# Kernel tuning notes

Measured on AMD Instinct MI355X. Metric: run time of the kernel, lower is better.

## Reference

```python
import jax, jax.numpy as jnp
import numpy as np

SX = 512; SY = 512; C = 3; NK = 10; R = 10
DT = 0.2; DD = 5; SIGMA = 0.65; THETA_A = 1.0; NPOW = 2


def setup_inputs() -> dict:
    rng = np.random.RandomState(0)
    r = rng.uniform(0.3, 1.0, NK).astype(np.float32)
    m = rng.uniform(0.05, 0.5, NK).astype(np.float32)
    s = rng.uniform(0.01, 0.18, NK).astype(np.float32)
    h = rng.uniform(0.2, 1.0, NK).astype(np.float32)
    a = rng.uniform(0.0, 1.0, (NK, 3)).astype(np.float32)
    w = rng.uniform(0.01, 0.5, (NK, 3)).astype(np.float32)
    b = rng.uniform(0.0, 1.0, (NK, 3)).astype(np.float32)
    # compute_kernel(): radial distance grid, ring sigmoid * sum-of-bumps ker_f, normalized
    mid = SX // 2
    x = np.linspace(-mid, mid, 2 * mid, dtype=np.float32)
    X, Y = np.meshgrid(x, x, indexing='ij')
    dist = np.sqrt(X ** 2 + Y ** 2)
    D = dist[:, :, None] / ((R + 15.0) * r)                      # (SX, SY, NK)
    ring = 1.0 / (1.0 + np.exp((D - 1.0) * 10.0))                # sigmoid(-(D-1)*10)
    bumps = (b * np.exp(-((D[..., None] - a) ** 2) / w)).sum(-1)  # ker_f(D, a, w, b)
    K = (ring * bumps).astype(np.float32)
    nK_ker = K / K.sum(axis=(0, 1), keepdims=True)               # (SX, SY, NK)
    # kernel -> source channel, and kernel -> target channel one-hot (c1 as matrix)
    c0 = np.array([0, 0, 0, 1, 1, 1, 2, 2, 2, 0], dtype=np.int32)
    tgt = np.array([0, 1, 2, 0, 1, 2, 0, 1, 2, 0], dtype=np.int32)
    c1_mat = np.zeros((NK, C), dtype=np.int32)
    c1_mat[np.arange(NK), tgt] = 1
    key = jax.random.key(0)
    A = jax.random.uniform(key, (SX, SY, C), dtype=jnp.float32)  # scale_init_state = 1
    return {"A": A, "nK_ker": jnp.asarray(nK_ker), "m": jnp.asarray(m),
            "s": jnp.asarray(s), "h": jnp.asarray(h),
            "c0": jnp.asarray(c0), "c1_mat": jnp.asarray(c1_mat)}


def _sobel(A):
    """A: (SX, SY, Cc) -> (SX, SY, 2, Cc), circular (toroidal) boundary."""
    def grad_ax(ax):
        sm_ax = 1 - ax
        sm = jnp.roll(A, 1, sm_ax) + 2.0 * A + jnp.roll(A, -1, sm_ax)  # [1,2,1] smoothing
        return (jnp.roll(sm, -1, ax) - jnp.roll(sm, 1, ax)) / 8.0       # central diff
    return jnp.stack([grad_ax(0), grad_ax(1)], axis=2)


def _flowlenia_step(A, nK_ker, m, s, h, c0, c1_mat):
    # FFT Lenia convolution
    fA = jnp.fft.fft2(A, axes=(0, 1))                              # (SX, SY, C) complex
    fK = jnp.fft.fft2(jnp.fft.fftshift(nK_ker, axes=(0, 1)), axes=(0, 1))
    U = jnp.real(jnp.fft.ifft2(fK * fA[:, :, c0], axes=(0, 1)))    # (SX, SY, NK)
    # growth * h, then gather-sum kernels into target channels (c1)
    U = (2.0 * jnp.exp(-((U - m) ** 2) / (2.0 * s ** 2)) - 1.0) * h
    U = jnp.einsum('xyk,kc->xyc', U, c1_mat.astype(U.dtype))       # (SX, SY, C)
    # flow field
    nabla_U = _sobel(U)                                            # (SX, SY, 2, C)
    nabla_A = _sobel(A.sum(-1, keepdims=True))                     # (SX, SY, 2, 1)
    alpha = jnp.clip((A[:, :, None, :] / THETA_A) ** NPOW, 0.0, 1.0)
    F = nabla_U * (1.0 - alpha) - nabla_A * alpha                  # (SX, SY, 2, C)
    # reintegration tracking (mass-conserving advection over (2*DD+1)^2 shifts)
    xs = jnp.arange(SX, dtype=A.dtype)
    ys = jnp.arange(SY, dtype=A.dtype)
    X, Y = jnp.meshgrid(xs, ys, indexing='ij')
    pos = jnp.stack([X, Y], axis=-1) + 0.5                         # (SX, SY, 2) cell centers
    ma = DD - SIGMA                                                # max flow magnitude
    mu = pos[..., None] + DT * jnp.clip(F, -ma, ma)                # (SX, SY, 2, C)
    shifts = jnp.array([(dx, dy) for dx in range(-DD, DD + 1)
                        for dy in range(-DD, DD + 1)], dtype=jnp.int32)
    clip_hi = min(1.0, 2.0 * SIGMA)
    inv_norm = 1.0 / (4.0 * SIGMA ** 2)

    def body(acc, sh):
        dx, dy = sh[0], sh[1]
        rA = jnp.roll(jnp.roll(A, dx, 0), dy, 1)
        rmu = jnp.roll(jnp.roll(mu, dx, 0), dy, 1)
        sz = 0.5 - jnp.abs(pos[..., None] - rmu) + SIGMA
        area = jnp.prod(jnp.clip(sz, 0.0, clip_hi), axis=2) * inv_norm  # (SX, SY, C)
        return acc + rA * area, None

    nA, _ = jax.lax.scan(body, jnp.zeros_like(A), shifts)
    return nA


def reference(A, nK_ker, m, s, h, c0, c1_mat):
    return _flowlenia_step(A, nK_ker, m, s, h, c0, c1_mat)
```

## Files before the change

kernel.cpp:

```cpp
#include <hip/hip_runtime.h>
#include <math.h>

#define NF 512
#define NF2 (NF * NF)
#define RPB 4
#define ROWLEN 580
#define PI_F 3.14159265358979323846f

#define LPAD(q) ((q) + ((q) >> 3))

__device__ inline float2 cadd(float2 a, float2 b) { return make_float2(a.x + b.x, a.y + b.y); }
__device__ inline float2 csub(float2 a, float2 b) { return make_float2(a.x - b.x, a.y - b.y); }
__device__ inline float2 cmul(float2 a, float2 b) {
    return make_float2(a.x * b.x - a.y * b.y, a.x * b.y + a.y * b.x);
}

__device__ inline void fft8(float2 x[8], float dsign) {
    const float s = 0.70710678118654752440f;
    float2 a0 = cadd(x[0], x[4]), a1 = cadd(x[1], x[5]);
    float2 a2 = cadd(x[2], x[6]), a3 = cadd(x[3], x[7]);
    float2 b0 = csub(x[0], x[4]), b1 = csub(x[1], x[5]);
    float2 b2 = csub(x[2], x[6]), b3 = csub(x[3], x[7]);
    b1 = cmul(b1, make_float2(s, dsign * s));
    b2 = make_float2(-dsign * b2.y, dsign * b2.x);
    b3 = cmul(b3, make_float2(-s, dsign * s));
    float2 c0 = cadd(a0, a2), c1 = cadd(a1, a3);
    float2 c2 = csub(a0, a2), c3 = csub(a1, a3);
    c3 = make_float2(-dsign * c3.y, dsign * c3.x);
    float2 d0 = cadd(b0, b2), d1 = cadd(b1, b3);
    float2 d2 = csub(b0, b2), d3 = csub(b1, b3);
    d3 = make_float2(-dsign * d3.y, dsign * d3.x);
    x[0] = cadd(c0, c1); x[4] = csub(c0, c1);
    x[2] = cadd(c2, c3); x[6] = csub(c2, c3);
    x[1] = cadd(d0, d1); x[5] = csub(d0, d1);
    x[3] = cadd(d2, d3); x[7] = csub(d2, d3);
}

__device__ inline void twiddle8(float2 x[8], float2 wb) {
    float2 tw = wb;
    x[1] = cmul(x[1], tw); tw = cmul(tw, wb);
    x[2] = cmul(x[2], tw); tw = cmul(tw, wb);
    x[3] = cmul(x[3], tw); tw = cmul(tw, wb);
    x[4] = cmul(x[4], tw); tw = cmul(tw, wb);
    x[5] = cmul(x[5], tw); tw = cmul(tw, wb);
    x[6] = cmul(x[6], tw); tw = cmul(tw, wb);
    x[7] = cmul(x[7], tw);
}

__device__ inline void fft512_regs(float2 x[8], int b, float2* bufA, float2* bufB,
                                   const float2* Wt, float dsign) {
    fft8(x, dsign);
    float2 wb0 = make_float2(Wt[b].x, dsign * Wt[b].y);
    twiddle8(x, wb0);
#pragma unroll
    for (int p = 0; p < 8; ++p) bufA[9 * b + p] = x[p];
    __syncthreads();
#pragma unroll
    for (int j = 0; j < 8; ++j) x[j] = bufA[LPAD(b + 64 * j)];
    fft8(x, dsign);
    int u = b >> 3, v = b & 7;
    float2 wb1 = make_float2(Wt[b & ~7].x, dsign * Wt[b & ~7].y);
    twiddle8(x, wb1);
    int base = u * 64 + v;
#pragma unroll
    for (int p = 0; p < 8; ++p) bufB[LPAD(base + 8 * p)] = x[p];
    __syncthreads();
#pragma unroll
    for (int j = 0; j < 8; ++j) x[j] = bufB[LPAD(b + 64 * j)];
    fft8(x, dsign);
}

#define FFT_PRE                                                    \
    __shared__ float2 SHA[RPB][ROWLEN];                            \
    __shared__ float2 SHB[RPB][ROWLEN];                            \
    __shared__ float2 Wt[512];                                     \
    int tid = threadIdx.x;                                         \
    int rr_ = tid >> 6, bb_ = tid & 63;                            \
    {                                                              \
        float sn, cs;                                              \
        sincosf((PI_F / 256.0f) * (float)tid, &sn, &cs);           \
        Wt[tid] = make_float2(cs, sn);                             \
        sincosf((PI_F / 256.0f) * (float)(tid + 256), &sn, &cs);   \
        Wt[tid + 256] = make_float2(cs, sn);                       \
    }

__global__ __launch_bounds__(256) void k_fwd_p1(const float* __restrict__ A,
                                                const float* __restrict__ K,
                                                float2* __restrict__ Z) {
    FFT_PRE
    int pl = blockIdx.y;
    const float* bre; int sre, cre;
    const float* bim; int sim, cim;
    switch (pl) {
        case 0: bre = A; sre = 3; cre = 0; bim = A; sim = 3; cim = 1; break;
        case 1: bre = A; sre = 3; cre = 2; bim = K; sim = 10; cim = 0; break;
        case 2: bre = K; sre = 10; cre = 1; bim = K; sim = 10; cim = 2; break;
        case 3: bre = K; sre = 10; cre = 3; bim = K; sim = 10; cim = 4; break;
        case 4: bre = K; sre = 10; cre = 5; bim = K; sim = 10; cim = 6; break;
        case 5: bre = K; sre = 10; cre = 7; bim = K; sim = 10; cim = 8; break;
        default: bre = K; sre = 10; cre = 9; bim = nullptr; sim = 0; cim = 0; break;
    }
    int x0 = blockIdx.x * RPB;
    int row = x0 + rr_;
    float2 x[8];
#pragma unroll
    for (int j = 0; j < 8; ++j) {
        int idx = (row << 9) + bb_ + 64 * j;
        float vr = bre[idx * sre + cre];
        float vi = bim ? bim[idx * sim + cim] : 0.0f;
        x[j] = make_float2(vr, vi);
    }
    __syncthreads();
    fft512_regs(x, bb_, &SHA[rr_][0], &SHB[rr_][0], Wt, -1.0f);
#pragma unroll
    for (int p2 = 0; p2 < 8; ++p2) SHA[rr_][LPAD(64 * p2 + bb_)] = x[p2];
    __syncthreads();
    for (int i = tid; i < RPB * NF; i += 256) {
        int r2 = i & (RPB - 1), ky = i >> 2;
        Z[(size_t)((pl << 9) + ky) * NF + x0 + r2] = SHA[r2][LPAD(ky)];
    }
}

__global__ __launch_bounds__(512) void k_rows_mul(const float2* __restrict__ Z,
                                                  const int* __restrict__ c0,
                                                  float2* __restrict__ tmpT) {
    __shared__ float2 RS[14][NF];
    __shared__ float2 SCA[8][ROWLEN];
    __shared__ float2 SCB[8][ROWLEN];
    __shared__ float2 Wt[512];
    int tid = threadIdx.x;
    int rr_ = tid >> 6, bb_ = tid & 63;
    {
        float sn, cs;
        sincosf((PI_F / 256.0f) * (float)tid, &sn, &cs);
        Wt[tid] = make_float2(cs, sn);
    }
    int b = blockIdx.x;
    bool selfm = (b == 0);
    int r1 = selfm ? 0 : b;
    int r2 = selfm ? 256 : NF - b;
    __syncthreads();

    for (int batch = 0; batch < 2; ++batch) {
        int ridx = batch * 8 + rr_;
        int rc = ridx < 14 ? ridx : 13;
        int p = rc >> 1, sl = rc & 1;
        int row = sl ? r2 : r1;
        float2 x[8];
        size_t base = (size_t)((p << 9) + row) * NF;
#pragma unroll
        for (int jj = 0; jj < 8; ++jj) x[jj] = Z[base + bb_ + 64 * jj];
        fft512_regs(x, bb_, &SCA[rr_][0], &SCB[rr_][0], Wt, -1.0f);
        if (ridx < 14) {
#pragma unroll
            for (int pp = 0; pp < 8; ++pp) RS[ridx][64 * pp + bb_] = x[pp];
        }
    }
    __syncthreads();

    for (int batch = 0; batch < 2; ++batch) {
        int q = batch * 8 + rr_;
        int qc = q < 10 ? q : 8;
        int j = qc >> 1, sl = qc & 1;
        int k1 = 2 * j, k2 = 2 * j + 1;
        int pK1 = (k1 == 0) ? 1 : 2 + ((k1 - 1) >> 1);
        int sK1 = (k1 == 0) ? 1 : ((k1 - 1) & 1);
        int pK2 = 2 + ((k2 - 1) >> 1);
        int sK2 = (k2 - 1) & 1;
        int cA1 = c0[k1], cA2 = c0[k2];
        int pA1 = cA1 >> 1, sA1 = cA1 & 1;
        int pA2 = cA2 >> 1, sA2 = cA2 & 1;
        int mo = selfm ? sl : (1 - sl);
        float2 x[8];
#pragma unroll
        for (int jj = 0; jj < 8; ++jj) {
            int kx = bb_ + 64 * jj;
            int mkx = (NF - kx) & (NF - 1);
            float2 zr, zm, fk1, fk2, fa1, fa2;
            zr = RS[2 * pK1 + sl][kx]; zm = RS[2 * pK1 + mo][mkx];
            fk1 = sK1 == 0 ? make_float2(0.5f * (zr.x + zm.x), 0.5f * (zr.y - zm.y))
                           : make_float2(0.5f * (zr.y + zm.y), 0.5f * (zm.x - zr.x));
            zr = RS[2 * pK2 + sl][kx]; zm = RS[2 * pK2 + mo][mkx];
            fk2 = sK2 == 0 ? make_float2(0.5f * (zr.x + zm.x), 0.5f * (zr.y - zm.y))
                           : make_float2(0.5f * (zr.y + zm.y), 0.5f * (zm.x - zr.x));
            zr = RS[2 * pA1 + sl][kx]; zm = RS[2 * pA1 + mo][mkx];
            fa1 = sA1 == 0 ? make_float2(0.5f * (zr.x + zm.x), 0.5f * (zr.y - zm.y))
                           : make_float2(0.5f * (zr.y + zm.y), 0.5f * (zm.x - zr.x));
            if (cA2 == cA1) fa2 = fa1;
            else {
                zr = RS[2 * pA2 + sl][kx]; zm = RS[2 * pA2 + mo][mkx];
                fa2 = sA2 == 0 ? make_float2(0.5f * (zr.x + zm.x), 0.5f * (zr.y - zm.y))
                               : make_float2(0.5f * (zr.y + zm.y), 0.5f * (zm.x - zr.x));
            }
            float t1x = fk1.x * fa1.x - fk1.y * fa1.y;
            float t1y = fk1.x * fa1.y + fk1.y * fa1.x;
            float t2x = fk2.x * fa2.x - fk2.y * fa2.y;
            float t2y = fk2.x * fa2.y + fk2.y * fa2.x;
            float sgn = ((kx + b) & 1) ? -1.0f : 1.0f;
            x[jj] = make_float2((t1x - t2y) * sgn, (t1y + t2x) * sgn);
        }
        fft512_regs(x, bb_, &SCA[rr_][0], &SCB[rr_][0], Wt, +1.0f);
        if (q < 10) {
            int orow = sl ? r2 : r1;
            size_t obase = ((size_t)j * NF + orow) * NF;
#pragma unroll
            for (int pp = 0; pp < 8; ++pp) tmpT[obase + 64 * pp + bb_] = x[pp];
        }
    }
}

__global__ __launch_bounds__(256) void k_inv_p2g(const float2* __restrict__ tmpT,
                                                 const float* __restrict__ mm,
                                                 const float* __restrict__ ss,
                                                 const float* __restrict__ hh,
                                                 float* __restrict__ G) {
    __shared__ float2 SH[4][NF];
    __shared__ float2 SCA[4][ROWLEN];
    __shared__ float2 SCB[4][ROWLEN];
    __shared__ float2 Wt[512];
    int tid = threadIdx.x;
    int rr_ = tid >> 6, bb_ = tid & 63;
    {
        float sn, cs;
        sincosf((PI_F / 256.0f) * (float)tid, &sn, &cs);
        Wt[tid] = make_float2(cs, sn);
        sincosf((PI_F / 256.0f) * (float)(tid + 256), &sn, &cs);
        Wt[tid + 256] = make_float2(cs, sn);
    }
    int j = blockIdx.y;
    int x0 = blockIdx.x * 4;
    for (int t = tid; t < NF; t += 256) {
        const float2* src = tmpT + ((size_t)j * NF + t) * NF + x0;
        float4 v0 = *(const float4*)(src);
        float4 v1 = *(const float4*)(src + 2);
        SH[0][t] = make_float2(v0.x, v0.y);
        SH[1][t] = make_float2(v0.z, v0.w);
        SH[2][t] = make_float2(v1.x, v1.y);
        SH[3][t] = make_float2(v1.z, v1.w);
    }
    __syncthreads();
    float2 x[8];
#pragma unroll
    for (int jj = 0; jj < 8; ++jj) x[jj] = SH[rr_][bb_ + 64 * jj];
    fft512_regs(x, bb_, &SCA[rr_][0], &SCB[rr_][0], Wt, +1.0f);
    int k1 = 2 * j, k2 = 2 * j + 1;
    float m1 = mm[k1], s1 = ss[k1], h1 = hh[k1];
    float m2 = mm[k2], s2 = ss[k2], h2 = hh[k2];
    float i2s1 = 1.0f / (2.0f * s1 * s1);
    float i2s2 = 1.0f / (2.0f * s2 * s2);
    const float scale = 1.0f / ((float)NF * (float)NF);
    int xcol = x0 + rr_;
#pragma unroll
    for (int p2 = 0; p2 < 8; ++p2) {
        int y = 64 * p2 + bb_;
        float u1 = x[p2].x * scale, u2 = x[p2].y * scale;
        float d1 = u1 - m1, d2 = u2 - m2;
        size_t o = (size_t)xcol * NF + y;
        G[(size_t)k1 * NF2 + o] = (2.0f * expf(-d1 * d1 * i2s1) - 1.0f) * h1;
        G[(size_t)k2 * NF2 + o] = (2.0f * expf(-d2 * d2 * i2s2) - 1.0f) * h2;
    }
}

#define HT 38
#define HT2 (HT * HT)
#define CT 36
#define CT2 (CT * CT)
__global__ __launch_bounds__(256) void k_tail(const float* __restrict__ G,
                                              const int* __restrict__ c1,
                                              const float* __restrict__ A,
                                              float* __restrict__ out) {
    __shared__ float sUp[3][HT2];
    __shared__ float sAs[HT2];
    __shared__ float sA[3][HT2];
    __shared__ float sM[6][CT2];
    int tid = threadIdx.x;
    int X0 = blockIdx.x * 32, Y0 = blockIdx.y * 32;

    float w0[10], w1[10], w2[10];
#pragma unroll
    for (int k = 0; k < 10; ++k) {
        w0[k] = (float)c1[k * 3 + 0];
        w1[k] = (float)c1[k * 3 + 1];
        w2[k] = (float)c1[k * 3 + 2];
    }

    for (int i = tid; i < HT2; i += 256) {
        int lx = i / HT, ly = i - lx * HT;
        int xg = (X0 - 3 + lx) & (NF - 1);
        int yg = (Y0 - 3 + ly) & (NF - 1);
        int gid = xg * NF + yg;
        float a0 = 0.f, a1 = 0.f, a2 = 0.f;
#pragma unroll
        for (int k = 0; k < 10; ++k) {
            float g = G[(size_t)k * NF2 + gid];
            a0 += g * w0[k]; a1 += g * w1[k]; a2 += g * w2[k];
        }
        sUp[0][i] = a0; sUp[1][i] = a1; sUp[2][i] = a2;
        float A0 = A[gid * 3 + 0], A1 = A[gid * 3 + 1], A2 = A[gid * 3 + 2];
        sA[0][i] = A0; sA[1][i] = A1; sA[2][i] = A2;
        sAs[i] = A0 + A1 + A2;
    }
    __syncthreads();

    for (int i = tid; i < CT2; i += 256) {
        int lx = i / CT, ly = i - lx * CT;
        int ci = (lx + 1) * HT + (ly + 1);
        int xg = (X0 - 2 + lx) & (NF - 1);
        int yg = (Y0 - 2 + ly) & (NF - 1);

        auto grad38 = [&](const float* f, float& gx, float& gy) {
            float fmm = f[ci - HT - 1], fm0 = f[ci - HT], fmp = f[ci - HT + 1];
            float f0m = f[ci - 1], f0p = f[ci + 1];
            float fpm = f[ci + HT - 1], fp0 = f[ci + HT], fpp = f[ci + HT + 1];
            gx = (fpm + 2.0f * fp0 + fpp - fmm - 2.0f * fm0 - fmp) * 0.125f;
            gy = (fmp + 2.0f * f0p + fpp - fmm - 2.0f * f0m - fpm) * 0.125f;
        };
        float gax, gay;
        grad38(sAs, gax, gay);
        float px = (float)xg + 0.5f, py = (float)yg + 0.5f;
#pragma unroll
        for (int c = 0; c < 3; ++c) {
            float gux, guy;
            grad38(sUp[c], gux, guy);
            float a = sA[c][ci];
            float al = fminf(a * a, 1.0f);
            float Fx = gux * (1.0f - al) - gax * al;
            float Fy = guy * (1.0f - al) - gay * al;
            Fx = fminf(fmaxf(Fx, -4.35f), 4.35f);
            Fy = fminf(fmaxf(Fy, -4.35f), 4.35f);
            sM[c][i] = px + 0.2f * Fx;
            sM[3 + c][i] = py + 0.2f * Fy;
        }
    }
    __syncthreads();

    const float INV_NORM = (float)(1.0 / (4.0 * 0.65 * 0.65));
    int cy = tid & 31, cx0 = tid >> 5;
    for (int sidx = 0; sidx < 4; ++sidx) {
        int cx = cx0 + 8 * sidx;
        int x = X0 + cx, y = Y0 + cy;
        float px = (float)x + 0.5f, py = (float)y + 0.5f;
        float acc0 = 0.f, acc1 = 0.f, acc2 = 0.f;
#pragma unroll
        for (int dx = 0; dx < 5; ++dx)
#pragma unroll
            for (int dy = 0; dy < 5; ++dy) {
                int li36 = (cx + dx) * CT + (cy + dy);
                int li38 = (cx + dx + 1) * HT + (cy + dy + 1);
#pragma unroll
                for (int c = 0; c < 3; ++c) {
                    float mux = sM[c][li36], muy = sM[3 + c][li36];
                    float szx = 0.5f - fabsf(px - mux) + 0.65f;
                    float szy = 0.5f - fabsf(py - muy) + 0.65f;
                    szx = fminf(fmaxf(szx, 0.0f), 1.0f);
                    szy = fminf(fmaxf(szy, 0.0f), 1.0f);
                    float area = szx * szy * INV_NORM;
                    float v = sA[c][li38] * area;
                    if (c == 0) acc0 += v;
                    else if (c == 1) acc1 += v;
                    else acc2 += v;
                }
            }
        int gid = x * NF + y;
        out[gid * 3 + 0] = acc0;
        out[gid * 3 + 1] = acc1;
        out[gid * 3 + 2] = acc2;
    }
}

extern "C" void kernel_launch(void* const* d_in, const int* in_sizes, int n_in,
                              void* d_out, int out_size, void* d_ws, size_t ws_size,
                              hipStream_t stream) {
    (void)in_sizes; (void)n_in; (void)out_size; (void)ws_size;
    const float* A  = (const float*)d_in[0];
    const float* nK = (const float*)d_in[1];
    const float* m  = (const float*)d_in[2];
    const float* s  = (const float*)d_in[3];
    const float* h  = (const float*)d_in[4];
    const int*   c0 = (const int*)d_in[5];
    const int*   c1 = (const int*)d_in[6];
    float* out = (float*)d_out;

    char* ws = (char*)d_ws;
    float2* Z    = (float2*)ws;
    float2* tmpT = (float2*)(ws + 14680064);
    float*  G    = (float*)ws;

    k_fwd_p1<<<dim3(NF / RPB, 7), dim3(256), 0, stream>>>(A, nK, Z);
    k_rows_mul<<<dim3(256), dim3(512), 0, stream>>>(Z, c0, tmpT);
    k_inv_p2g<<<dim3(NF / 4, 5), dim3(256), 0, stream>>>(tmpT, m, s, h, G);
    k_tail<<<dim3(16, 16), dim3(256), 0, stream>>>(G, c1, A, out);
}
```

Before: 130.0 us.

## Fuse four FFT-conv stages into one cooperative persistent kernel with grid syncs

Merges the forward column FFT, row FFT plus spectral multiply and inverse, inverse column FFT with growth mapping, and the advection tail into one cooperative kernel of 256 blocks of 512 threads. Stages are separated by grid.sync() and share one set of shared-memory buffers. This removes three kernel launches and their inter-kernel gaps. In exchange, stages that were launched with more or smaller blocks now run on only 256 blocks, so parallelism and occupancy drop, and each grid barrier has its own cost.

```diff
diff --git a/kernel.cpp b/kernel.cpp
--- a/kernel.cpp
+++ b/kernel.cpp
@@ -1,9 +1,11 @@
 #include <hip/hip_runtime.h>
+#include <hip/hip_cooperative_groups.h>
 #include <math.h>
+
+namespace cg = cooperative_groups;
 
 #define NF 512
 #define NF2 (NF * NF)
-#define RPB 4
 #define ROWLEN 580
 #define PI_F 3.14159265358979323846f
 
@@ -58,10 +60,9 @@
 #pragma unroll
     for (int j = 0; j < 8; ++j) x[j] = bufA[LPAD(b + 64 * j)];
     fft8(x, dsign);
-    int u = b >> 3, v = b & 7;
     float2 wb1 = make_float2(Wt[b & ~7].x, dsign * Wt[b & ~7].y);
     twiddle8(x, wb1);
-    int base = u * 64 + v;
+    int base = (b >> 3) * 64 + (b & 7);
 #pragma unroll
     for (int p = 0; p < 8; ++p) bufB[LPAD(base + 8 * p)] = x[p];
     __syncthreads();
@@ -70,301 +71,297 @@
     fft8(x, dsign);
 }
 
-#define FFT_PRE                                                    \
-    __shared__ float2 SHA[RPB][ROWLEN];                            \
-    __shared__ float2 SHB[RPB][ROWLEN];                            \
-    __shared__ float2 Wt[512];                                     \
-    int tid = threadIdx.x;                                         \
-    int rr_ = tid >> 6, bb_ = tid & 63;                            \
-    {                                                              \
-        float sn, cs;                                              \
-        sincosf((PI_F / 256.0f) * (float)tid, &sn, &cs);           \
-        Wt[tid] = make_float2(cs, sn);                             \
-        sincosf((PI_F / 256.0f) * (float)(tid + 256), &sn, &cs);   \
-        Wt[tid + 256] = make_float2(cs, sn);                       \
-    }
-
-__global__ __launch_bounds__(256) void k_fwd_p1(const float* __restrict__ A,
-                                                const float* __restrict__ K,
-                                                float2* __restrict__ Z) {
-    FFT_PRE
-    int pl = blockIdx.y;
-    const float* bre; int sre, cre;
-    const float* bim; int sim, cim;
-    switch (pl) {
-        case 0: bre = A; sre = 3; cre = 0; bim = A; sim = 3; cim = 1; break;
-        case 1: bre = A; sre = 3; cre = 2; bim = K; sim = 10; cim = 0; break;
-        case 2: bre = K; sre = 10; cre = 1; bim = K; sim = 10; cim = 2; break;
-        case 3: bre = K; sre = 10; cre = 3; bim = K; sim = 10; cim = 4; break;
-        case 4: bre = K; sre = 10; cre = 5; bim = K; sim = 10; cim = 6; break;
-        case 5: bre = K; sre = 10; cre = 7; bim = K; sim = 10; cim = 8; break;
-        default: bre = K; sre = 10; cre = 9; bim = nullptr; sim = 0; cim = 0; break;
-    }
-    int x0 = blockIdx.x * RPB;
-    int row = x0 + rr_;
-    float2 x[8];
-#pragma unroll
-    for (int j = 0; j < 8; ++j) {
-        int idx = (row << 9) + bb_ + 64 * j;
-        float vr = bre[idx * sre + cre];
-        float vi = bim ? bim[idx * sim + cim] : 0.0f;
-        x[j] = make_float2(vr, vi);
-    }
-    __syncthreads();
-    fft512_regs(x, bb_, &SHA[rr_][0], &SHB[rr_][0], Wt, -1.0f);
-#pragma unroll
-    for (int p2 = 0; p2 < 8; ++p2) SHA[rr_][LPAD(64 * p2 + bb_)] = x[p2];
-    __syncthreads();
-    for (int i = tid; i < RPB * NF; i += 256) {
-        int r2 = i & (RPB - 1), ky = i >> 2;
-        Z[(size_t)((pl << 9) + ky) * NF + x0 + r2] = SHA[r2][LPAD(ky)];
-    }
-}
-
-__global__ __launch_bounds__(512) void k_rows_mul(const float2* __restrict__ Z,
-                                                  const int* __restrict__ c0,
-                                                  float2* __restrict__ tmpT) {
+#define HT 38
+#define HT2 (HT * HT)
+#define CT 36
+#define CT2 (CT * CT)
+
+__global__ __launch_bounds__(512) void k_mega(const float* __restrict__ A,
+                                              const float* __restrict__ K,
+                                              const float* __restrict__ mm,
+                                              const float* __restrict__ ss,
+                                              const float* __restrict__ hh,
+                                              const int* __restrict__ c0,
+                                              const int* __restrict__ c1,
+                                              float2* __restrict__ Z,
+                                              float2* __restrict__ tmpT,
+                                              float* __restrict__ G,
+                                              float* __restrict__ out) {
     __shared__ float2 RS[14][NF];
     __shared__ float2 SCA[8][ROWLEN];
     __shared__ float2 SCB[8][ROWLEN];
     __shared__ float2 Wt[512];
+    cg::grid_group grid = cg::this_grid();
     int tid = threadIdx.x;
     int rr_ = tid >> 6, bb_ = tid & 63;
+    int blk = blockIdx.x;
     {
         float sn, cs;
         sincosf((PI_F / 256.0f) * (float)tid, &sn, &cs);
         Wt[tid] = make_float2(cs, sn);
     }
-    int b = blockIdx.x;
-    bool selfm = (b == 0);
-    int r1 = selfm ? 0 : b;
-    int r2 = selfm ? 256 : NF - b;
     __syncthreads();
 
-    for (int batch = 0; batch < 2; ++batch) {
-        int ridx = batch * 8 + rr_;
-        int rc = ridx < 14 ? ridx : 13;
-        int p = rc >> 1, sl = rc & 1;
-        int row = sl ? r2 : r1;
+    for (int t = 0; t < 2; ++t) {
+        int c = t * 256 + blk;
+        int cc = c < 448 ? c : 447;
+        int p = cc >> 6;
+        int x0 = (cc & 63) << 3;
+        int row = x0 + rr_;
+        const float* bre; int sre, cre;
+        const float* bim; int sim, cim;
+        switch (p) {
+            case 0: bre = A; sre = 3; cre = 0; bim = A; sim = 3; cim = 1; break;
+            case 1: bre = A; sre = 3; cre = 2; bim = K; sim = 10; cim = 0; break;
+            case 2: bre = K; sre = 10; cre = 1; bim = K; sim = 10; cim = 2; break;
+            case 3: bre = K; sre = 10; cre = 3; bim = K; sim = 10; cim = 4; break;
+            case 4: bre = K; sre = 10; cre = 5; bim = K; sim = 10; cim = 6; break;
+            case 5: bre = K; sre = 10; cre = 7; bim = K; sim = 10; cim = 8; break;
+            default: bre = K; sre = 10; cre = 9; bim = nullptr; sim = 0; cim = 0; break;
+        }
         float2 x[8];
-        size_t base = (size_t)((p << 9) + row) * NF;
-#pragma unroll
-        for (int jj = 0; jj < 8; ++jj) x[jj] = Z[base + bb_ + 64 * jj];
+#pragma unroll
+        for (int j = 0; j < 8; ++j) {
+            int idx = (row << 9) + bb_ + 64 * j;
+            float vr = bre[idx * sre + cre];
+            float vi = bim ? bim[idx * sim + cim] : 0.0f;
+            x[j] = make_float2(vr, vi);
+        }
         fft512_regs(x, bb_, &SCA[rr_][0], &SCB[rr_][0], Wt, -1.0f);
-        if (ridx < 14) {
-#pragma unroll
-            for (int pp = 0; pp < 8; ++pp) RS[ridx][64 * pp + bb_] = x[pp];
-        }
-    }
-    __syncthreads();
-
-    for (int batch = 0; batch < 2; ++batch) {
-        int q = batch * 8 + rr_;
-        int qc = q < 10 ? q : 8;
-        int j = qc >> 1, sl = qc & 1;
-        int k1 = 2 * j, k2 = 2 * j + 1;
-        int pK1 = (k1 == 0) ? 1 : 2 + ((k1 - 1) >> 1);
-        int sK1 = (k1 == 0) ? 1 : ((k1 - 1) & 1);
-        int pK2 = 2 + ((k2 - 1) >> 1);
-        int sK2 = (k2 - 1) & 1;
-        int cA1 = c0[k1], cA2 = c0[k2];
-        int pA1 = cA1 >> 1, sA1 = cA1 & 1;
-        int pA2 = cA2 >> 1, sA2 = cA2 & 1;
-        int mo = selfm ? sl : (1 - sl);
+#pragma unroll
+        for (int p2 = 0; p2 < 8; ++p2) SCA[rr_][LPAD(64 * p2 + bb_)] = x[p2];
+        __syncthreads();
+        if (c < 448) {
+            for (int i = tid; i < 8 * NF; i += 512) {
+                int r2 = i & 7, ky = i >> 3;
+                Z[(size_t)((p << 9) + ky) * NF + x0 + r2] = SCA[r2][LPAD(ky)];
+            }
+        }
+        __syncthreads();
+    }
+    grid.sync();
+
+    {
+        int b = blk;
+        bool selfm = (b == 0);
+        int r1 = selfm ? 0 : b;
+        int r2 = selfm ? 256 : NF - b;
+        for (int batch = 0; batch < 2; ++batch) {
+            int ridx = batch * 8 + rr_;
+            int rc = ridx < 14 ? ridx : 13;
+            int p = rc >> 1, sl = rc & 1;
+            int row = sl ? r2 : r1;
+            float2 x[8];
+            size_t base = (size_t)((p << 9) + row) * NF;
+#pragma unroll
+            for (int jj = 0; jj < 8; ++jj) x[jj] = Z[base + bb_ + 64 * jj];
+            fft512_regs(x, bb_, &SCA[rr_][0], &SCB[rr_][0], Wt, -1.0f);
+            if (ridx < 14) {
+#pragma unroll
+                for (int pp = 0; pp < 8; ++pp) RS[ridx][64 * pp + bb_] = x[pp];
+            }
+        }
+        __syncthreads();
+        for (int batch = 0; batch < 2; ++batch) {
+            int q = batch * 8 + rr_;
+            int qc = q < 10 ? q : 8;
+            int j = qc >> 1, sl = qc & 1;
+            int k1 = 2 * j, k2 = 2 * j + 1;
+            int pK1 = (k1 == 0) ? 1 : 2 + ((k1 - 1) >> 1);
+            int sK1 = (k1 == 0) ? 1 : ((k1 - 1) & 1);
+            int pK2 = 2 + ((k2 - 1) >> 1);
+            int sK2 = (k2 - 1) & 1;
+            int cA1 = c0[k1], cA2 = c0[k2];
+            int pA1 = cA1 >> 1, sA1 = cA1 & 1;
+            int pA2 = cA2 >> 1, sA2 = cA2 & 1;
+            int mo = selfm ? sl : (1 - sl);
+            float2 x[8];
+#pragma unroll
+            for (int jj = 0; jj < 8; ++jj) {
+                int kx = bb_ + 64 * jj;
+                int mkx = (NF - kx) & (NF - 1);
+                float2 zr, zm, fk1, fk2, fa1, fa2;
+                zr = RS[2 * pK1 + sl][kx]; zm = RS[2 * pK1 + mo][mkx];
+                fk1 = sK1 == 0 ? make_float2(0.5f * (zr.x + zm.x), 0.5f * (zr.y - zm.y))
+                               : make_float2(0.5f * (zr.y + zm.y), 0.5f * (zm.x - zr.x));
+                zr = RS[2 * pK2 + sl][kx]; zm = RS[2 * pK2 + mo][mkx];
+                fk2 = sK2 == 0 ? make_float2(0.5f * (zr.x + zm.x), 0.5f * (zr.y - zm.y))
+                               : make_float2(0.5f * (zr.y + zm.y), 0.5f * (zm.x - zr.x));
+                zr = RS[2 * pA1 + sl][kx]; zm = RS[2 * pA1 + mo][mkx];
+                fa1 = sA1 == 0 ? make_float2(0.5f * (zr.x + zm.x), 0.5f * (zr.y - zm.y))
+                               : make_float2(0.5f * (zr.y + zm.y), 0.5f * (zm.x - zr.x));
+                if (cA2 == cA1) fa2 = fa1;
+                else {
+                    zr = RS[2 * pA2 + sl][kx]; zm = RS[2 * pA2 + mo][mkx];
+                    fa2 = sA2 == 0 ? make_float2(0.5f * (zr.x + zm.x), 0.5f * (zr.y - zm.y))
+                                   : make_float2(0.5f * (zr.y + zm.y), 0.5f * (zm.x - zr.x));
+                }
+                float t1x = fk1.x * fa1.x - fk1.y * fa1.y;
+                float t1y = fk1.x * fa1.y + fk1.y * fa1.x;
+                float t2x = fk2.x * fa2.x - fk2.y * fa2.y;
+                float t2y = fk2.x * fa2.y + fk2.y * fa2.x;
+                float sgn = ((kx + b) & 1) ? -1.0f : 1.0f;
+                x[jj] = make_float2((t1x - t2y) * sgn, (t1y + t2x) * sgn);
+            }
+            fft512_regs(x, bb_, &SCA[rr_][0], &SCB[rr_][0], Wt, +1.0f);
+            if (q < 10) {
+                int orow = sl ? r2 : r1;
+                size_t obase = ((size_t)j * NF + orow) * NF;
+#pragma unroll
+                for (int pp = 0; pp < 8; ++pp) tmpT[obase + 64 * pp + bb_] = x[pp];
+            }
+        }
+    }
+    grid.sync();
+
+    for (int t = 0; t < 2; ++t) {
+        int qb = t * 2048 + blk * 8;
+        bool valid = qb < 2560;
+        int qbc = valid ? qb : 2552;
+        int j = qbc >> 9;
+        int x0 = qbc & 511;
+        {
+            const float2* src = tmpT + ((size_t)j * NF + tid) * NF + x0;
+            float4 v0 = *(const float4*)(src + 0);
+            float4 v1 = *(const float4*)(src + 2);
+            float4 v2 = *(const float4*)(src + 4);
+            float4 v3 = *(const float4*)(src + 6);
+            RS[0][tid] = make_float2(v0.x, v0.y); RS[1][tid] = make_float2(v0.z, v0.w);
+            RS[2][tid] = make_float2(v1.x, v1.y); RS[3][tid] = make_float2(v1.z, v1.w);
+            RS[4][tid] = make_float2(v2.x, v2.y); RS[5][tid] = make_float2(v2.z, v2.w);
+            RS[6][tid] = make_float2(v3.x, v3.y); RS[7][tid] = make_float2(v3.z, v3.w);
+        }
+        __syncthreads();
         float2 x[8];
 #pragma unroll
-        for (int jj = 0; jj < 8; ++jj) {
-            int kx = bb_ + 64 * jj;
-            int mkx = (NF - kx) & (NF - 1);
-            float2 zr, zm, fk1, fk2, fa1, fa2;
-            zr = RS[2 * pK1 + sl][kx]; zm = RS[2 * pK1 + mo][mkx];
-            fk1 = sK1 == 0 ? make_float2(0.5f * (zr.x + zm.x), 0.5f * (zr.y - zm.y))
-                           : make_float2(0.5f * (zr.y + zm.y), 0.5f * (zm.x - zr.x));
-            zr = RS[2 * pK2 + sl][kx]; zm = RS[2 * pK2 + mo][mkx];
-            fk2 = sK2 == 0 ? make_float2(0.5f * (zr.x + zm.x), 0.5f * (zr.y - zm.y))
-                           : make_float2(0.5f * (zr.y + zm.y), 0.5f * (zm.x - zr.x));
-            zr = RS[2 * pA1 + sl][kx]; zm = RS[2 * pA1 + mo][mkx];
-            fa1 = sA1 == 0 ? make_float2(0.5f * (zr.x + zm.x), 0.5f * (zr.y - zm.y))
-                           : make_float2(0.5f * (zr.y + zm.y), 0.5f * (zm.x - zr.x));
-            if (cA2 == cA1) fa2 = fa1;
-            else {
-                zr = RS[2 * pA2 + sl][kx]; zm = RS[2 * pA2 + mo][mkx];
-                fa2 = sA2 == 0 ? make_float2(0.5f * (zr.x + zm.x), 0.5f * (zr.y - zm.y))
-                               : make_float2(0.5f * (zr.y + zm.y), 0.5f * (zm.x - zr.x));
-            }
-            float t1x = fk1.x * fa1.x - fk1.y * fa1.y;
-            float t1y = fk1.x * fa1.y + fk1.y * fa1.x;
-            float t2x = fk2.x * fa2.x - fk2.y * fa2.y;
-            float t2y = fk2.x * fa2.y + fk2.y * fa2.x;
-            float sgn = ((kx + b) & 1) ? -1.0f : 1.0f;
-            x[jj] = make_float2((t1x - t2y) * sgn, (t1y + t2x) * sgn);
-        }
+        for (int jj = 0; jj < 8; ++jj) x[jj] = RS[rr_][bb_ + 64 * jj];
         fft512_regs(x, bb_, &SCA[rr_][0], &SCB[rr_][0], Wt, +1.0f);
-        if (q < 10) {
-            int orow = sl ? r2 : r1;
-            size_t obase = ((size_t)j * NF + orow) * NF;
-#pragma unroll
-            for (int pp = 0; pp < 8; ++pp) tmpT[obase + 64 * pp + bb_] = x[pp];
-        }
-    }
-}
-
-__global__ __launch_bounds__(256) void k_inv_p2g(const float2* __restrict__ tmpT,
-                                                 const float* __restrict__ mm,
-                                                 const float* __restrict__ ss,
-                                                 const float* __restrict__ hh,
-                                                 float* __restrict__ G) {
-    __shared__ float2 SH[4][NF];
-    __shared__ float2 SCA[4][ROWLEN];
-    __shared__ float2 SCB[4][ROWLEN];
-    __shared__ float2 Wt[512];
-    int tid = threadIdx.x;
-    int rr_ = tid >> 6, bb_ = tid & 63;
+        if (valid) {
+            int k1 = 2 * j, k2 = 2 * j + 1;
+            float m1 = mm[k1], s1 = ss[k1], h1 = hh[k1];
+            float m2 = mm[k2], s2 = ss[k2], h2 = hh[k2];
+            float i2s1 = 1.0f / (2.0f * s1 * s1);
+            float i2s2 = 1.0f / (2.0f * s2 * s2);
+            const float scale = 1.0f / ((float)NF * (float)NF);
+            int xcol = x0 + rr_;
+#pragma unroll
+            for (int p2 = 0; p2 < 8; ++p2) {
+                int y = 64 * p2 + bb_;
+                float u1 = x[p2].x * scale, u2 = x[p2].y * scale;
+                float d1 = u1 - m1, d2 = u2 - m2;
+                size_t o = (size_t)xcol * NF + y;
+                G[(size_t)k1 * NF2 + o] = (2.0f * expf(-d1 * d1 * i2s1) - 1.0f) * h1;
+                G[(size_t)k2 * NF2 + o] = (2.0f * expf(-d2 * d2 * i2s2) - 1.0f) * h2;
+            }
+        }
+        __syncthreads();
+    }
+    grid.sync();
+
     {
-        float sn, cs;
-        sincosf((PI_F / 256.0f) * (float)tid, &sn, &cs);
-        Wt[tid] = make_float2(cs, sn);
-        sincosf((PI_F / 256.0f) * (float)(tid + 256), &sn, &cs);
-        Wt[tid + 256] = make_float2(cs, sn);
-    }
-    int j = blockIdx.y;
-    int x0 = blockIdx.x * 4;
-    for (int t = tid; t < NF; t += 256) {
-        const float2* src = tmpT + ((size_t)j * NF + t) * NF + x0;
-        float4 v0 = *(const float4*)(src);
-        float4 v1 = *(const float4*)(src + 2);
-        SH[0][t] = make_float2(v0.x, v0.y);
-        SH[1][t] = make_float2(v0.z, v0.w);
-        SH[2][t] = make_float2(v1.x, v1.y);
-        SH[3][t] = make_float2(v1.z, v1.w);
-    }
-    __syncthreads();
-    float2 x[8];
-#pragma unroll
-    for (int jj = 0; jj < 8; ++jj) x[jj] = SH[rr_][bb_ + 64 * jj];
-    fft512_regs(x, bb_, &SCA[rr_][0], &SCB[rr_][0], Wt, +1.0f);
-    int k1 = 2 * j, k2 = 2 * j + 1;
-    float m1 = mm[k1], s1 = ss[k1], h1 = hh[k1];
-    float m2 = mm[k2], s2 = ss[k2], h2 = hh[k2];
-    float i2s1 = 1.0f / (2.0f * s1 * s1);
-    float i2s2 = 1.0f / (2.0f * s2 * s2);
-    const float scale = 1.0f / ((float)NF * (float)NF);
-    int xcol = x0 + rr_;
-#pragma unroll
-    for (int p2 = 0; p2 < 8; ++p2) {
-        int y = 64 * p2 + bb_;
-        float u1 = x[p2].x * scale, u2 = x[p2].y * scale;
-        float d1 = u1 - m1, d2 = u2 - m2;
-        size_t o = (size_t)xcol * NF + y;
-        G[(size_t)k1 * NF2 + o] = (2.0f * expf(-d1 * d1 * i2s1) - 1.0f) * h1;
-        G[(size_t)k2 * NF2 + o] = (2.0f * expf(-d2 * d2 * i2s2) - 1.0f) * h2;
-    }
-}
-
-#define HT 38
-#define HT2 (HT * HT)
-#define CT 36
-#define CT2 (CT * CT)
-__global__ __launch_bounds__(256) void k_tail(const float* __restrict__ G,
-                                              const int* __restrict__ c1,
-                                              const float* __restrict__ A,
-                                              float* __restrict__ out) {
-    __shared__ float sUp[3][HT2];
-    __shared__ float sAs[HT2];
-    __shared__ float sA[3][HT2];
-    __shared__ float sM[6][CT2];
-    int tid = threadIdx.x;
-    int X0 = blockIdx.x * 32, Y0 = blockIdx.y * 32;
-
-    float w0[10], w1[10], w2[10];
-#pragma unroll
-    for (int k = 0; k < 10; ++k) {
-        w0[k] = (float)c1[k * 3 + 0];
-        w1[k] = (float)c1[k * 3 + 1];
-        w2[k] = (float)c1[k * 3 + 2];
-    }
-
-    for (int i = tid; i < HT2; i += 256) {
-        int lx = i / HT, ly = i - lx * HT;
-        int xg = (X0 - 3 + lx) & (NF - 1);
-        int yg = (Y0 - 3 + ly) & (NF - 1);
-        int gid = xg * NF + yg;
-        float a0 = 0.f, a1 = 0.f, a2 = 0.f;
+        float* sUp0 = (float*)&RS[0][0];
+        float* sUp1 = sUp0 + HT2;
+        float* sUp2 = sUp1 + HT2;
+        float* sAs  = sUp2 + HT2;
+        float* sA0  = sAs + HT2;
+        float* sA1  = sA0 + HT2;
+        float* sA2  = sA1 + HT2;
+        float* sM   = (float*)&SCA[0][0];
+        int X0 = (blk >> 4) * 32, Y0 = (blk & 15) * 32;
+
+        float w0[10], w1[10], w2[10];
 #pragma unroll
         for (int k = 0; k < 10; ++k) {
-            float g = G[(size_t)k * NF2 + gid];
-            a0 += g * w0[k]; a1 += g * w1[k]; a2 += g * w2[k];
-        }
-        sUp[0][i] = a0; sUp[1][i] = a1; sUp[2][i] = a2;
-        float A0 = A[gid * 3 + 0], A1 = A[gid * 3 + 1], A2 = A[gid * 3 + 2];
-        sA[0][i] = A0; sA[1][i] = A1; sA[2][i] = A2;
-        sAs[i] = A0 + A1 + A2;
-    }
-    __syncthreads();
-
-    for (int i = tid; i < CT2; i += 256) {
-        int lx = i / CT, ly = i - lx * CT;
-        int ci = (lx + 1) * HT + (ly + 1);
-        int xg = (X0 - 2 + lx) & (NF - 1);
-        int yg = (Y0 - 2 + ly) & (NF - 1);
-
-        auto grad38 = [&](const float* f, float& gx, float& gy) {
-            float fmm = f[ci - HT - 1], fm0 = f[ci - HT], fmp = f[ci - HT + 1];
-            float f0m = f[ci - 1], f0p = f[ci + 1];
-            float fpm = f[ci + HT - 1], fp0 = f[ci + HT], fpp = f[ci + HT + 1];
-            gx = (fpm + 2.0f * fp0 + fpp - fmm - 2.0f * fm0 - fmp) * 0.125f;
-            gy = (fmp + 2.0f * f0p + fpp - fmm - 2.0f * f0m - fpm) * 0.125f;
-        };
-        float gax, gay;
-        grad38(sAs, gax, gay);
-        float px = (float)xg + 0.5f, py = (float)yg + 0.5f;
-#pragma unroll
-        for (int c = 0; c < 3; ++c) {
-            float gux, guy;
-            grad38(sUp[c], gux, guy);
-            float a = sA[c][ci];
-            float al = fminf(a * a, 1.0f);
-            float Fx = gux * (1.0f - al) - gax * al;
-            float Fy = guy * (1.0f - al) - gay * al;
-            Fx = fminf(fmaxf(Fx, -4.35f), 4.35f);
-            Fy = fminf(fmaxf(Fy, -4.35f), 4.35f);
-            sM[c][i] = px + 0.2f * Fx;
-            sM[3 + c][i] = py + 0.2f * Fy;
-        }
-    }
-    __syncthreads();
-
-    const float INV_NORM = (float)(1.0 / (4.0 * 0.65 * 0.65));
-    int cy = tid & 31, cx0 = tid >> 5;
-    for (int sidx = 0; sidx < 4; ++sidx) {
-        int cx = cx0 + 8 * sidx;
-        int x = X0 + cx, y = Y0 + cy;
-        float px = (float)x + 0.5f, py = (float)y + 0.5f;
-        float acc0 = 0.f, acc1 = 0.f, acc2 = 0.f;
-#pragma unroll
-        for (int dx = 0; dx < 5; ++dx)
-#pragma unroll
-            for (int dy = 0; dy < 5; ++dy) {
-                int li36 = (cx + dx) * CT + (cy + dy);
-                int li38 = (cx + dx + 1) * HT + (cy + dy + 1);
-#pragma unroll
-                for (int c = 0; c < 3; ++c) {
-                    float mux = sM[c][li36], muy = sM[3 + c][li36];
-                    float szx = 0.5f - fabsf(px - mux) + 0.65f;
-                    float szy = 0.5f - fabsf(py - muy) + 0.65f;
-                    szx = fminf(fmaxf(szx, 0.0f), 1.0f);
-                    szy = fminf(fmaxf(szy, 0.0f), 1.0f);
-                    float area = szx * szy * INV_NORM;
-                    float v = sA[c][li38] * area;
-                    if (c == 0) acc0 += v;
-                    else if (c == 1) acc1 += v;
-                    else acc2 += v;
+            w0[k] = (float)c1[k * 3 + 0];
+            w1[k] = (float)c1[k * 3 + 1];
+            w2[k] = (float)c1[k * 3 + 2];
+        }
+
+        for (int i = tid; i < HT2; i += 512) {
+            int lx = i / HT, ly = i - lx * HT;
+            int xg = (X0 - 3 + lx) & (NF - 1);
+            int yg = (Y0 - 3 + ly) & (NF - 1);
+            int gid = xg * NF + yg;
+            float a0 = 0.f, a1 = 0.f, a2 = 0.f;
+#pragma unroll
+            for (int k = 0; k < 10; ++k) {
+                float g = G[(size_t)k * NF2 + gid];
+                a0 += g * w0[k]; a1 += g * w1[k]; a2 += g * w2[k];
+            }
+            sUp0[i] = a0; sUp1[i] = a1; sUp2[i] = a2;
+            float A0 = A[gid * 3 + 0], A1 = A[gid * 3 + 1], A2 = A[gid * 3 + 2];
+            sA0[i] = A0; sA1[i] = A1; sA2[i] = A2;
+            sAs[i] = A0 + A1 + A2;
+        }
+        __syncthreads();
+
+        for (int i = tid; i < CT2; i += 512) {
+            int lx = i / CT, ly = i - lx * CT;
+            int ci = (lx + 1) * HT + (ly + 1);
+            int xg = (X0 - 2 + lx) & (NF - 1);
+            int yg = (Y0 - 2 + ly) & (NF - 1);
+
+            auto grad38 = [&](const float* f, float& gx, float& gy) {
+                float fmm = f[ci - HT - 1], fm0 = f[ci - HT], fmp = f[ci - HT + 1];
+                float f0m = f[ci - 1], f0p = f[ci + 1];
+                float fpm = f[ci + HT - 1], fp0 = f[ci + HT], fpp = f[ci + HT + 1];
+                gx = (fpm + 2.0f * fp0 + fpp - fmm - 2.0f * fm0 - fmp) * 0.125f;
+                gy = (fmp + 2.0f * f0p + fpp - fmm - 2.0f * f0m - fpm) * 0.125f;
+            };
+            float gax, gay;
+            grad38(sAs, gax, gay);
+            float px = (float)xg + 0.5f, py = (float)yg + 0.5f;
+            const float* sUpc[3] = {sUp0, sUp1, sUp2};
+            const float* sAc[3] = {sA0, sA1, sA2};
+#pragma unroll
+            for (int c = 0; c < 3; ++c) {
+                float gux, guy;
+                grad38(sUpc[c], gux, guy);
+                float a = sAc[c][ci];
+                float al = fminf(a * a, 1.0f);
+                float Fx = gux * (1.0f - al) - gax * al;
+                float Fy = guy * (1.0f - al) - gay * al;
+                Fx = fminf(fmaxf(Fx, -4.35f), 4.35f);
+                Fy = fminf(fmaxf(Fy, -4.35f), 4.35f);
+                sM[c * CT2 + i] = px + 0.2f * Fx;
+                sM[(3 + c) * CT2 + i] = py + 0.2f * Fy;
+            }
+        }
+        __syncthreads();
+
+        const float INV_NORM = (float)(1.0 / (4.0 * 0.65 * 0.65));
+        int cy = tid & 31, cx0 = tid >> 5;
+        const float* sAc[3] = {sA0, sA1, sA2};
+        for (int sidx = 0; sidx < 2; ++sidx) {
+            int cx = cx0 + 16 * sidx;
+            int x = X0 + cx, y = Y0 + cy;
+            float px = (float)x + 0.5f, py = (float)y + 0.5f;
+            float acc0 = 0.f, acc1 = 0.f, acc2 = 0.f;
+#pragma unroll
+            for (int dx = 0; dx < 5; ++dx)
+#pragma unroll
+                for (int dy = 0; dy < 5; ++dy) {
+                    int li36 = (cx + dx) * CT + (cy + dy);
+                    int li38 = (cx + dx + 1) * HT + (cy + dy + 1);
+#pragma unroll
+                    for (int c = 0; c < 3; ++c) {
+                        float mux = sM[c * CT2 + li36], muy = sM[(3 + c) * CT2 + li36];
+                        float szx = 0.5f - fabsf(px - mux) + 0.65f;
+                        float szy = 0.5f - fabsf(py - muy) + 0.65f;
+                        szx = fminf(fmaxf(szx, 0.0f), 1.0f);
+                        szy = fminf(fmaxf(szy, 0.0f), 1.0f);
+                        float area = szx * szy * INV_NORM;
+                        float v = sAc[c][li38] * area;
+                        if (c == 0) acc0 += v;
+                        else if (c == 1) acc1 += v;
+                        else acc2 += v;
+                    }
                 }
-            }
-        int gid = x * NF + y;
-        out[gid * 3 + 0] = acc0;
-        out[gid * 3 + 1] = acc1;
-        out[gid * 3 + 2] = acc2;
+            int gid = x * NF + y;
+            out[gid * 3 + 0] = acc0;
+            out[gid * 3 + 1] = acc1;
+            out[gid * 3 + 2] = acc2;
+        }
     }
 }
 
@@ -386,8 +383,8 @@
     float2* tmpT = (float2*)(ws + 14680064);
     float*  G    = (float*)ws;
 
-    k_fwd_p1<<<dim3(NF / RPB, 7), dim3(256), 0, stream>>>(A, nK, Z);
-    k_rows_mul<<<dim3(256), dim3(512), 0, stream>>>(Z, c0, tmpT);
-    k_inv_p2g<<<dim3(NF / 4, 5), dim3(256), 0, stream>>>(tmpT, m, s, h, G);
-    k_tail<<<dim3(16, 16), dim3(256), 0, stream>>>(G, c1, A, out);
-}
+    void* args[] = {(void*)&A, (void*)&nK, (void*)&m, (void*)&s, (void*)&h,
+                    (void*)&c0, (void*)&c1, (void*)&Z, (void*)&tmpT, (void*)&G,
+                    (void*)&out};
+    hipLaunchCooperativeKernel((const void*)k_mega, dim3(256), dim3(512), args, 0, stream);
+}
```

Measured after the change: 232.9 us. 1.79x slower.
